# Kernel optimization log

Hardware: AMD Instinct MI355X
Metric: run time of the kernel (lower is better)

The kernel has to match this reference:

```python
import jax, jax.numpy as jnp
import numpy as np

B, C, HH, WW = 16, 512, 32, 32
NUM_HEADS = 8
NUM_GROUPS = 32
EPS = 1e-5


def setup_inputs() -> dict:
    key = jax.random.key(0)
    ks = jax.random.split(key, 4)
    x = jax.random.normal(ks[0], (B, C, HH, WW), dtype=jnp.float32)
    gn_scale = jnp.ones((C,), dtype=jnp.float32)
    gn_bias = jnp.zeros((C,), dtype=jnp.float32)
    qkv_w = jax.random.normal(ks[1], (3 * C, C), dtype=jnp.float32) * (1.0 / np.sqrt(C))
    qkv_b = jnp.zeros((3 * C,), dtype=jnp.float32)
    # NOTE: original zero-inits proj_out; we use random weights for a non-trivial baseline.
    proj_w = jax.random.normal(ks[2], (C, C), dtype=jnp.float32) * (1.0 / np.sqrt(C))
    proj_b = jnp.zeros((C,), dtype=jnp.float32)
    return {"x": x, "gn_scale": gn_scale, "gn_bias": gn_bias,
            "qkv_w": qkv_w, "qkv_b": qkv_b, "proj_w": proj_w, "proj_b": proj_b}


def reference(x, gn_scale, gn_bias, qkv_w, qkv_b, proj_w, proj_b):
    b, c, h, w = x.shape
    t = h * w
    nh = NUM_HEADS
    d = c // nh
    xf = x.reshape(b, c, t)                      # (B, C, T)

    # GroupNorm(32, C) over (channels-in-group, spatial)
    xg = xf.reshape(b, NUM_GROUPS, (c // NUM_GROUPS) * t)
    mu = jnp.mean(xg, axis=-1, keepdims=True)
    var = jnp.var(xg, axis=-1, keepdims=True)
    xn = ((xg - mu) * jax.lax.rsqrt(var + EPS)).reshape(b, c, t)
    xn = xn * gn_scale[:, None] + gn_bias[:, None]

    # 1x1 conv QKV: (3C, C) matmul over channel dim
    qkv = jnp.einsum('oc,bct->bot', qkv_w, xn) + qkv_b[:, None]
    # channel axis splits as (3, H, D) per rearrange 'B (three H C) T -> three B T H C'
    qkv = qkv.reshape(b, 3, nh, d, t)
    q, k, v = qkv[:, 0], qkv[:, 1], qkv[:, 2]    # each (B, H, D, T)

    scale = 1.0 / jnp.sqrt(jnp.asarray(d, x.dtype))
    logits = jnp.einsum('bhdt,bhds->bhts', q, k) * scale   # (B, H, T, S)
    probs = jax.nn.softmax(logits, axis=-1)
    attn = jnp.einsum('bhts,bhds->bhdt', probs, v)         # (B, H, D, T)

    hout = attn.reshape(b, c, t)                 # 'B T H C -> B (H C) T'
    hout = jnp.einsum('oc,bct->bot', proj_w, hout) + proj_b[:, None]
    return (hout + xf).reshape(b, c, h, w)
```

## Files before the change

### kernel.cpp

```cpp
#include <hip/hip_runtime.h>

typedef unsigned short ushort_t;
typedef unsigned int uint_t;
typedef __bf16 bf16x8 __attribute__((ext_vector_type(8)));
typedef float f32x4 __attribute__((ext_vector_type(4)));
typedef uint_t u32x4 __attribute__((ext_vector_type(4)));
typedef uint_t u32x2 __attribute__((ext_vector_type(2)));


static __device__ __forceinline__ ushort_t f2bf(float f) {
  union { float f; uint_t u; } v; v.f = f;
  uint_t r = v.u + 0x7FFFu + ((v.u >> 16) & 1u);
  return (ushort_t)(r >> 16);
}

static __device__ __forceinline__ uint_t cvt_pk_bf16(float lo, float hi) {
  uint_t r;
  asm("v_cvt_pk_bf16_f32 %0, %1, %2" : "=v"(r) : "v"(lo), "v"(hi));
  return r;
}

static __device__ __forceinline__ f32x4 mfma_bf16(bf16x8 a, bf16x8 b, f32x4 c) {
  return __builtin_amdgcn_mfma_f32_16x16x32_bf16(a, b, c, 0, 0, 0);
}

__global__ __launch_bounds__(256) void k_convert(const float* __restrict__ src,
                                                 ushort_t* __restrict__ dst, int n) {
  int i = (blockIdx.x * 256 + threadIdx.x) * 4;
  if (i >= n) return;
  f32x4 v = *(const f32x4*)(src + i);
  u32x2 o;
  o[0] = (uint_t)f2bf(v[0]) | ((uint_t)f2bf(v[1]) << 16);
  o[1] = (uint_t)f2bf(v[2]) | ((uint_t)f2bf(v[3]) << 16);
  *(u32x2*)(dst + i) = o;
}

__global__ __launch_bounds__(256) void k_gn(const float* __restrict__ x,
                                            const float* __restrict__ gsc,
                                            const float* __restrict__ gbi,
                                            ushort_t* __restrict__ xnT) {
  const int g = blockIdx.x, b = blockIdx.y;
  const int tid = threadIdx.x;
  const float* xp = x + ((size_t)b * 512 + g * 16) * 1024;

  float s = 0.f, q = 0.f;
#pragma unroll
  for (int i = 0; i < 16; ++i) {
    f32x4 v = *(const f32x4*)(xp + (tid + i * 256) * 4);
    s += v[0] + v[1] + v[2] + v[3];
    q += v[0]*v[0] + v[1]*v[1] + v[2]*v[2] + v[3]*v[3];
  }
#pragma unroll
  for (int off = 32; off > 0; off >>= 1) { s += __shfl_xor(s, off); q += __shfl_xor(q, off); }

  __shared__ float rs[4], rq[4], ssc[16], sbi[16], stats[2];
  if ((tid & 63) == 0) { rs[tid >> 6] = s; rq[tid >> 6] = q; }
  if (tid < 16) { ssc[tid] = gsc[g * 16 + tid]; sbi[tid] = gbi[g * 16 + tid]; }
  __syncthreads();
  if (tid == 0) {
    float S = rs[0] + rs[1] + rs[2] + rs[3];
    float Q = rq[0] + rq[1] + rq[2] + rq[3];
    float mean = S * (1.f / 16384.f);
    float var  = Q * (1.f / 16384.f) - mean * mean;
    stats[0] = mean; stats[1] = rsqrtf(var + 1e-5f);
  }
  __syncthreads();
  const float mean = stats[0], rstd = stats[1];

#pragma unroll
  for (int i = 0; i < 8; ++i) {
    int u = tid + i * 256;
    int t = u >> 1, half = u & 1;
    union { ushort_t us[8]; u32x4 v4; } o;
#pragma unroll
    for (int j = 0; j < 8; ++j) {
      int c = half * 8 + j;
      float v = (xp[(size_t)c * 1024 + t] - mean) * rstd * ssc[c] + sbi[c];
      o.us[j] = f2bf(v);
    }
    *(u32x4*)(xnT + ((size_t)b * 1024 + t) * 512 + g * 16 + half * 8) = o.v4;
  }
}

__global__ __launch_bounds__(256) void k_qkv(const ushort_t* __restrict__ xnT,
                                             const ushort_t* __restrict__ Wbf,
                                             const float* __restrict__ bias,
                                             ushort_t* __restrict__ qkT,
                                             ushort_t* __restrict__ vbuf) {
  const int mi = blockIdx.x, ni = blockIdx.y, b = blockIdx.z;
  const int tid = threadIdx.x, lane = tid & 63, w = tid >> 6;
  const int wm = w >> 1, wn = w & 1;
  const int lr = lane & 15, lg = lane >> 4;

  __shared__ __align__(16) ushort_t As[128 * 40];
  __shared__ __align__(16) ushort_t Bs[128 * 40];
  __shared__ __align__(16) float tbuf[32 * 132];

  const ushort_t* Ap = xnT + (size_t)b * 1024 * 512 + (size_t)mi * 128 * 512;
  const ushort_t* Bp = Wbf + (size_t)ni * 128 * 512;

  f32x4 acc[4][4] = {};

  for (int kt = 0; kt < 16; ++kt) {
    const int k0 = kt * 32;
#pragma unroll
    for (int uu = 0; uu < 2; ++uu) {
      const int u = tid + uu * 256;
      const int row = u >> 2, seg = u & 3;
      const u32x4 av = *(const u32x4*)(Ap + (size_t)row * 512 + k0 + seg * 8);
      const u32x4 bv = *(const u32x4*)(Bp + (size_t)row * 512 + k0 + seg * 8);
      *(u32x4*)(As + row * 40 + seg * 8) = av;
      *(u32x4*)(Bs + row * 40 + seg * 8) = bv;
    }
    __syncthreads();
    bf16x8 af[4], bfv[4];
#pragma unroll
    for (int i = 0; i < 4; ++i)
      af[i] = *(const bf16x8*)(As + (wm * 64 + i * 16 + lr) * 40 + lg * 8);
#pragma unroll
    for (int j = 0; j < 4; ++j)
      bfv[j] = *(const bf16x8*)(Bs + (wn * 64 + j * 16 + lr) * 40 + lg * 8);
    __builtin_amdgcn_s_setprio(1);
#pragma unroll
    for (int i = 0; i < 4; ++i)
#pragma unroll
      for (int j = 0; j < 4; ++j)
        acc[i][j] = mfma_bf16(af[i], bfv[j], acc[i][j]);
    __builtin_amdgcn_s_setprio(0);
    __syncthreads();
  }

  float biasv[4];
#pragma unroll
  for (int j = 0; j < 4; ++j) biasv[j] = bias[ni * 128 + wn * 64 + j * 16 + lr];

  if (ni < 8) {
    const float oscale = (ni >= 4) ? 0.1803368801f : 1.0f;
    ushort_t* outp = qkT + ((size_t)b * 1024 + mi * 128) * 1024 + ni * 128;
#pragma unroll
    for (int i = 0; i < 4; ++i)
#pragma unroll
      for (int j = 0; j < 4; ++j)
#pragma unroll
        for (int r = 0; r < 4; ++r) {
          const int m = wm * 64 + i * 16 + lg * 4 + r;
          const int n = wn * 64 + j * 16 + lr;
          outp[(size_t)m * 1024 + n] = f2bf((acc[i][j][r] + biasv[j]) * oscale);
        }
  } else {
    ushort_t* tb = (ushort_t*)tbuf;
#pragma unroll
    for (int c = 0; c < 4; ++c) {
      if (wn == (c >> 1)) {
#pragma unroll
        for (int jj = 0; jj < 2; ++jj) {
          const int j = (c & 1) * 2 + jj;
#pragma unroll
          for (int i = 0; i < 4; ++i)
#pragma unroll
            for (int r = 0; r < 4; ++r) {
              const int m = wm * 64 + i * 16 + lg * 4 + r;
              const int nl = jj * 16 + lr;
              tb[nl * 136 + m] = f2bf(acc[i][j][r] + biasv[j]);
            }
        }
      }
      __syncthreads();
      for (int u = tid; u < 512; u += 256) {
        const int nl = u >> 4, seg = u & 15;
        const int op = ni * 128 + c * 32 + nl - 1024;
        *(u32x4*)(vbuf + ((size_t)b * 512 + op) * 1024 + mi * 128 + seg * 8) =
            *(const u32x4*)(tb + nl * 136 + seg * 8);
      }
      __syncthreads();
    }
  }
}

#define PSTR 68
__global__ __launch_bounds__(256) void k_attn(const ushort_t* __restrict__ qkT,
                                              const ushort_t* __restrict__ vbuf,
                                              ushort_t* __restrict__ attnT) {
  const int qt = blockIdx.x, h = blockIdx.y, b = blockIdx.z;
  const int tid = threadIdx.x, lane = tid & 63, w = tid >> 6;
  const int lr = lane & 15, lg = lane >> 4;

  __shared__ __align__(16) ushort_t Ks[64 * PSTR];
  __shared__ __align__(16) ushort_t Vs[64 * PSTR];
  __shared__ __align__(16) ushort_t Ps[4 * 32 * PSTR];

  bf16x8 aq[2][2];
#pragma unroll
  for (int tI = 0; tI < 2; ++tI) {
    const int t = qt * 128 + w * 32 + tI * 16 + lr;
    const ushort_t* qp = qkT + ((size_t)b * 1024 + t) * 1024 + h * 64 + lg * 8;
    aq[tI][0] = *(const bf16x8*)(qp);
    aq[tI][1] = *(const bf16x8*)(qp + 32);
  }

  f32x4 oacc[2][4] = {};
  float lrun[2][4] = {};

  const size_t vbase = ((size_t)b * 512 + h * 64) * 1024;
  ushort_t* Pw = Ps + w * 32 * PSTR;

  for (int st = 0; st < 16; ++st) {
    const int s0 = st * 64;
    __syncthreads();
#pragma unroll
    for (int uu = 0; uu < 2; ++uu) {
      const int u = tid + uu * 256;
      const int row = u >> 3, seg = u & 7;
      const u32x4 kv = *(const u32x4*)(qkT + ((size_t)b * 1024 + s0 + row) * 1024 + 512 + h * 64 + seg * 8);
      const u32x4 vv = *(const u32x4*)(vbuf + vbase + (size_t)row * 1024 + s0 + seg * 8);
      *(u32x4*)(Ks + row * PSTR + seg * 8) = kv;
      *(u32x4*)(Vs + row * PSTR + seg * 8) = vv;
    }
    __syncthreads();

    f32x4 sacc[2][4] = {};
    __builtin_amdgcn_s_setprio(1);
#pragma unroll
    for (int sI = 0; sI < 4; ++sI) {
      const bf16x8 bk0 = *(const bf16x8*)(Ks + (sI * 16 + lr) * PSTR + lg * 8);
      const bf16x8 bk1 = *(const bf16x8*)(Ks + (sI * 16 + lr) * PSTR + 32 + lg * 8);
#pragma unroll
      for (int tI = 0; tI < 2; ++tI) {
        sacc[tI][sI] = mfma_bf16(aq[tI][0], bk0, sacc[tI][sI]);
        sacc[tI][sI] = mfma_bf16(aq[tI][1], bk1, sacc[tI][sI]);
      }
    }
    __builtin_amdgcn_s_setprio(0);

#pragma unroll
    for (int tI = 0; tI < 2; ++tI)
#pragma unroll
      for (int sI = 0; sI < 4; ++sI)
#pragma unroll
        for (int r = 0; r < 4; ++r)
          sacc[tI][sI][r] = __builtin_amdgcn_exp2f(sacc[tI][sI][r]);
#pragma unroll
    for (int tI = 0; tI < 2; ++tI)
#pragma unroll
      for (int r = 0; r < 4; ++r)
        lrun[tI][r] += (sacc[tI][0][r] + sacc[tI][1][r]) + (sacc[tI][2][r] + sacc[tI][3][r]);

#pragma unroll
    for (int tI = 0; tI < 2; ++tI)
#pragma unroll
      for (int r = 0; r < 4; ++r) {
        const int rb = (tI * 16 + lg * 4 + r) * PSTR;
        const uint_t u0 = cvt_pk_bf16(sacc[tI][0][r], sacc[tI][1][r]);
        const uint_t u1 = cvt_pk_bf16(sacc[tI][2][r], sacc[tI][3][r]);
        Pw[rb + lr]      = (ushort_t)u0;
        Pw[rb + lr + 16] = (ushort_t)(u0 >> 16);
        Pw[rb + lr + 32] = (ushort_t)u1;
        Pw[rb + lr + 48] = (ushort_t)(u1 >> 16);
      }

#pragma unroll
    for (int tI = 0; tI < 2; ++tI) {
      const bf16x8 ap0 = *(const bf16x8*)(Pw + (tI * 16 + lr) * PSTR + lg * 8);
      const bf16x8 ap1 = *(const bf16x8*)(Pw + (tI * 16 + lr) * PSTR + 32 + lg * 8);
      __builtin_amdgcn_s_setprio(1);
#pragma unroll
      for (int dI = 0; dI < 4; ++dI) {
        const bf16x8 bv0 = *(const bf16x8*)(Vs + (dI * 16 + lr) * PSTR + lg * 8);
        const bf16x8 bv1 = *(const bf16x8*)(Vs + (dI * 16 + lr) * PSTR + 32 + lg * 8);
        oacc[tI][dI] = mfma_bf16(ap0, bv0, oacc[tI][dI]);
        oacc[tI][dI] = mfma_bf16(ap1, bv1, oacc[tI][dI]);
      }
      __builtin_amdgcn_s_setprio(0);
    }
  }

  float inv[2][4];
#pragma unroll
  for (int tI = 0; tI < 2; ++tI)
#pragma unroll
    for (int r = 0; r < 4; ++r) {
      float sum = lrun[tI][r];
      sum += __shfl_xor(sum, 1);
      sum += __shfl_xor(sum, 2);
      sum += __shfl_xor(sum, 4);
      sum += __shfl_xor(sum, 8);
      inv[tI][r] = 1.f / sum;
    }
#pragma unroll
  for (int tI = 0; tI < 2; ++tI)
#pragma unroll
    for (int dI = 0; dI < 4; ++dI)
#pragma unroll
      for (int r = 0; r < 4; ++r) {
        const int t = qt * 128 + w * 32 + tI * 16 + lg * 4 + r;
        attnT[((size_t)b * 1024 + t) * 512 + h * 64 + dI * 16 + lr] =
            f2bf(oacc[tI][dI][r] * inv[tI][r]);
      }
}

__global__ __launch_bounds__(256) void k_proj(const ushort_t* __restrict__ attnT,
                                              const ushort_t* __restrict__ Wbf,
                                              const float* __restrict__ bias,
                                              const float* __restrict__ xres,
                                              float* __restrict__ outp) {
  const int mi = blockIdx.x, ni = blockIdx.y, b = blockIdx.z;
  const int tid = threadIdx.x, lane = tid & 63, w = tid >> 6;
  const int wm = w >> 1, wn = w & 1;
  const int lr = lane & 15, lg = lane >> 4;

  __shared__ __align__(16) ushort_t As[128 * 40];
  __shared__ __align__(16) ushort_t Bs[128 * 40];
  __shared__ __align__(16) float tbuf[32 * 132];

  const ushort_t* Ap = attnT + (size_t)b * 1024 * 512 + (size_t)mi * 128 * 512;
  const ushort_t* Bp = Wbf + (size_t)ni * 128 * 512;

  f32x4 acc[4][4] = {};

  for (int kt = 0; kt < 16; ++kt) {
    const int k0 = kt * 32;
#pragma unroll
    for (int uu = 0; uu < 2; ++uu) {
      const int u = tid + uu * 256;
      const int row = u >> 2, seg = u & 3;
      const u32x4 av = *(const u32x4*)(Ap + (size_t)row * 512 + k0 + seg * 8);
      const u32x4 bv = *(const u32x4*)(Bp + (size_t)row * 512 + k0 + seg * 8);
      *(u32x4*)(As + row * 40 + seg * 8) = av;
      *(u32x4*)(Bs + row * 40 + seg * 8) = bv;
    }
    __syncthreads();
    bf16x8 af[4], bfv[4];
#pragma unroll
    for (int i = 0; i < 4; ++i)
      af[i] = *(const bf16x8*)(As + (wm * 64 + i * 16 + lr) * 40 + lg * 8);
#pragma unroll
    for (int j = 0; j < 4; ++j)
      bfv[j] = *(const bf16x8*)(Bs + (wn * 64 + j * 16 + lr) * 40 + lg * 8);
    __builtin_amdgcn_s_setprio(1);
#pragma unroll
    for (int i = 0; i < 4; ++i)
#pragma unroll
      for (int j = 0; j < 4; ++j)
        acc[i][j] = mfma_bf16(af[i], bfv[j], acc[i][j]);
    __builtin_amdgcn_s_setprio(0);
    __syncthreads();
  }

  float biasv[4];
#pragma unroll
  for (int j = 0; j < 4; ++j) biasv[j] = bias[ni * 128 + wn * 64 + j * 16 + lr];

#pragma unroll
  for (int c = 0; c < 4; ++c) {
    if (wn == (c >> 1)) {
#pragma unroll
      for (int jj = 0; jj < 2; ++jj) {
        const int j = (c & 1) * 2 + jj;
#pragma unroll
        for (int i = 0; i < 4; ++i)
#pragma unroll
          for (int r = 0; r < 4; ++r) {
            const int m = wm * 64 + i * 16 + lg * 4 + r;
            const int nl = jj * 16 + lr;
            tbuf[nl * 132 + m] = acc[i][j][r] + biasv[j];
          }
      }
    }
    __syncthreads();
    for (int u = tid; u < 1024; u += 256) {
      const int nl = u >> 5, seg = u & 31;
      const int o = ni * 128 + c * 32 + nl;
      const size_t idx = ((size_t)b * 512 + o) * 1024 + mi * 128 + seg * 4;
      const f32x4 t = *(const f32x4*)(tbuf + nl * 132 + seg * 4);
      const f32x4 xr = *(const f32x4*)(xres + idx);
      f32x4 ov = t + xr;
      *(f32x4*)(outp + idx) = ov;
    }
    __syncthreads();
  }
}

extern "C" void kernel_launch(void* const* d_in, const int* in_sizes, int n_in,
                              void* d_out, int out_size, void* d_ws, size_t ws_size,
                              hipStream_t stream) {
  (void)in_sizes; (void)n_in; (void)out_size; (void)ws_size;
  const float* x      = (const float*)d_in[0];
  const float* gsc    = (const float*)d_in[1];
  const float* gbi    = (const float*)d_in[2];
  const float* qkv_w  = (const float*)d_in[3];
  const float* qkv_b  = (const float*)d_in[4];
  const float* proj_w = (const float*)d_in[5];
  const float* proj_b = (const float*)d_in[6];
  float* out = (float*)d_out;

  char* ws = (char*)d_ws;
  ushort_t* xnT   = (ushort_t*)(ws);
  ushort_t* qkT   = (ushort_t*)(ws + 16777216);
  ushort_t* vbuf  = (ushort_t*)(ws + 50331648);
  ushort_t* attnT = (ushort_t*)(ws + 67108864);
  ushort_t* qwbf  = (ushort_t*)(ws + 83886080);
  ushort_t* pwbf  = (ushort_t*)(ws + 85458944);

  k_convert<<<768, 256, 0, stream>>>(qkv_w, qwbf, 1536 * 512);
  k_convert<<<256, 256, 0, stream>>>(proj_w, pwbf, 512 * 512);
  k_gn<<<dim3(32, 16), 256, 0, stream>>>(x, gsc, gbi, xnT);
  k_qkv<<<dim3(8, 12, 16), 256, 0, stream>>>(xnT, qwbf, qkv_b, qkT, vbuf);
  k_attn<<<dim3(8, 8, 16), 256, 0, stream>>>(qkT, vbuf, attnT);
  k_proj<<<dim3(8, 4, 16), 256, 0, stream>>>(attnT, pwbf, proj_b, x, out);
}
```

Measured before the change: 256.7 us.

## Register-prefetch next K/V and GEMM tiles to overlap global loads with MFMA

In the QKV GEMM, attention and projection kernels, the next tile's global loads are issued into registers before the current tile's MFMA work and written to shared memory afterwards. This hides global memory latency behind compute using a single LDS buffer with two barriers per iteration. It costs extra vector registers per thread, which may reduce occupancy in the attention kernel.

```diff
diff --git a/kernel.cpp b/kernel.cpp
--- a/kernel.cpp
+++ b/kernel.cpp
@@ -99,20 +99,29 @@
   const ushort_t* Ap = xnT + (size_t)b * 1024 * 512 + (size_t)mi * 128 * 512;
   const ushort_t* Bp = Wbf + (size_t)ni * 128 * 512;
 
+  const int row0 = tid >> 2, seg = tid & 3;
+  u32x4 ra0, ra1, rb0, rb1;
+
+  ra0 = *(const u32x4*)(Ap + (size_t)row0 * 512 + seg * 8);
+  ra1 = *(const u32x4*)(Ap + (size_t)(row0 + 64) * 512 + seg * 8);
+  rb0 = *(const u32x4*)(Bp + (size_t)row0 * 512 + seg * 8);
+  rb1 = *(const u32x4*)(Bp + (size_t)(row0 + 64) * 512 + seg * 8);
+  *(u32x4*)(As + row0 * 40 + seg * 8) = ra0;
+  *(u32x4*)(As + (row0 + 64) * 40 + seg * 8) = ra1;
+  *(u32x4*)(Bs + row0 * 40 + seg * 8) = rb0;
+  *(u32x4*)(Bs + (row0 + 64) * 40 + seg * 8) = rb1;
+  __syncthreads();
+
   f32x4 acc[4][4] = {};
 
   for (int kt = 0; kt < 16; ++kt) {
-    const int k0 = kt * 32;
-#pragma unroll
-    for (int uu = 0; uu < 2; ++uu) {
-      const int u = tid + uu * 256;
-      const int row = u >> 2, seg = u & 3;
-      const u32x4 av = *(const u32x4*)(Ap + (size_t)row * 512 + k0 + seg * 8);
-      const u32x4 bv = *(const u32x4*)(Bp + (size_t)row * 512 + k0 + seg * 8);
-      *(u32x4*)(As + row * 40 + seg * 8) = av;
-      *(u32x4*)(Bs + row * 40 + seg * 8) = bv;
-    }
-    __syncthreads();
+    if (kt < 15) {
+      const int k0n = (kt + 1) * 32;
+      ra0 = *(const u32x4*)(Ap + (size_t)row0 * 512 + k0n + seg * 8);
+      ra1 = *(const u32x4*)(Ap + (size_t)(row0 + 64) * 512 + k0n + seg * 8);
+      rb0 = *(const u32x4*)(Bp + (size_t)row0 * 512 + k0n + seg * 8);
+      rb1 = *(const u32x4*)(Bp + (size_t)(row0 + 64) * 512 + k0n + seg * 8);
+    }
     bf16x8 af[4], bfv[4];
 #pragma unroll
     for (int i = 0; i < 4; ++i)
@@ -127,7 +136,14 @@
       for (int j = 0; j < 4; ++j)
         acc[i][j] = mfma_bf16(af[i], bfv[j], acc[i][j]);
     __builtin_amdgcn_s_setprio(0);
-    __syncthreads();
+    if (kt < 15) {
+      __syncthreads();
+      *(u32x4*)(As + row0 * 40 + seg * 8) = ra0;
+      *(u32x4*)(As + (row0 + 64) * 40 + seg * 8) = ra1;
+      *(u32x4*)(Bs + row0 * 40 + seg * 8) = rb0;
+      *(u32x4*)(Bs + (row0 + 64) * 40 + seg * 8) = rb1;
+      __syncthreads();
+    }
   }
 
   float biasv[4];
@@ -167,10 +183,10 @@
       }
       __syncthreads();
       for (int u = tid; u < 512; u += 256) {
-        const int nl = u >> 4, seg = u & 15;
+        const int nl = u >> 4, sg = u & 15;
         const int op = ni * 128 + c * 32 + nl - 1024;
-        *(u32x4*)(vbuf + ((size_t)b * 512 + op) * 1024 + mi * 128 + seg * 8) =
-            *(const u32x4*)(tb + nl * 136 + seg * 8);
+        *(u32x4*)(vbuf + ((size_t)b * 512 + op) * 1024 + mi * 128 + sg * 8) =
+            *(const u32x4*)(tb + nl * 136 + sg * 8);
       }
       __syncthreads();
     }
@@ -202,21 +218,30 @@
   float lrun[2][4] = {};
 
   const size_t vbase = ((size_t)b * 512 + h * 64) * 1024;
+  const size_t kbase = (size_t)b * 1024 * 1024 + 512 + h * 64;
   ushort_t* Pw = Ps + w * 32 * PSTR;
 
+  const int srow = tid >> 3, sseg = tid & 7;
+  u32x4 kr0, kr1, vr0, vr1;
+
+  kr0 = *(const u32x4*)(qkT + kbase + (size_t)srow * 1024 + sseg * 8);
+  kr1 = *(const u32x4*)(qkT + kbase + (size_t)(srow + 32) * 1024 + sseg * 8);
+  vr0 = *(const u32x4*)(vbuf + vbase + (size_t)srow * 1024 + sseg * 8);
+  vr1 = *(const u32x4*)(vbuf + vbase + (size_t)(srow + 32) * 1024 + sseg * 8);
+  *(u32x4*)(Ks + srow * PSTR + sseg * 8) = kr0;
+  *(u32x4*)(Ks + (srow + 32) * PSTR + sseg * 8) = kr1;
+  *(u32x4*)(Vs + srow * PSTR + sseg * 8) = vr0;
+  *(u32x4*)(Vs + (srow + 32) * PSTR + sseg * 8) = vr1;
+  __syncthreads();
+
   for (int st = 0; st < 16; ++st) {
-    const int s0 = st * 64;
-    __syncthreads();
-#pragma unroll
-    for (int uu = 0; uu < 2; ++uu) {
-      const int u = tid + uu * 256;
-      const int row = u >> 3, seg = u & 7;
-      const u32x4 kv = *(const u32x4*)(qkT + ((size_t)b * 1024 + s0 + row) * 1024 + 512 + h * 64 + seg * 8);
-      const u32x4 vv = *(const u32x4*)(vbuf + vbase + (size_t)row * 1024 + s0 + seg * 8);
-      *(u32x4*)(Ks + row * PSTR + seg * 8) = kv;
-      *(u32x4*)(Vs + row * PSTR + seg * 8) = vv;
-    }
-    __syncthreads();
+    if (st < 15) {
+      const int s0n = (st + 1) * 64;
+      kr0 = *(const u32x4*)(qkT + kbase + (size_t)(s0n + srow) * 1024 + sseg * 8);
+      kr1 = *(const u32x4*)(qkT + kbase + (size_t)(s0n + srow + 32) * 1024 + sseg * 8);
+      vr0 = *(const u32x4*)(vbuf + vbase + (size_t)srow * 1024 + s0n + sseg * 8);
+      vr1 = *(const u32x4*)(vbuf + vbase + (size_t)(srow + 32) * 1024 + s0n + sseg * 8);
+    }
 
     f32x4 sacc[2][4] = {};
     __builtin_amdgcn_s_setprio(1);
@@ -271,6 +296,15 @@
         oacc[tI][dI] = mfma_bf16(ap1, bv1, oacc[tI][dI]);
       }
       __builtin_amdgcn_s_setprio(0);
+    }
+
+    if (st < 15) {
+      __syncthreads();
+      *(u32x4*)(Ks + srow * PSTR + sseg * 8) = kr0;
+      *(u32x4*)(Ks + (srow + 32) * PSTR + sseg * 8) = kr1;
+      *(u32x4*)(Vs + srow * PSTR + sseg * 8) = vr0;
+      *(u32x4*)(Vs + (srow + 32) * PSTR + sseg * 8) = vr1;
+      __syncthreads();
     }
   }
 
@@ -315,20 +349,29 @@
   const ushort_t* Ap = attnT + (size_t)b * 1024 * 512 + (size_t)mi * 128 * 512;
   const ushort_t* Bp = Wbf + (size_t)ni * 128 * 512;
 
+  const int row0 = tid >> 2, seg = tid & 3;
+  u32x4 ra0, ra1, rb0, rb1;
+
+  ra0 = *(const u32x4*)(Ap + (size_t)row0 * 512 + seg * 8);
+  ra1 = *(const u32x4*)(Ap + (size_t)(row0 + 64) * 512 + seg * 8);
+  rb0 = *(const u32x4*)(Bp + (size_t)row0 * 512 + seg * 8);
+  rb1 = *(const u32x4*)(Bp + (size_t)(row0 + 64) * 512 + seg * 8);
+  *(u32x4*)(As + row0 * 40 + seg * 8) = ra0;
+  *(u32x4*)(As + (row0 + 64) * 40 + seg * 8) = ra1;
+  *(u32x4*)(Bs + row0 * 40 + seg * 8) = rb0;
+  *(u32x4*)(Bs + (row0 + 64) * 40 + seg * 8) = rb1;
+  __syncthreads();
+
   f32x4 acc[4][4] = {};
 
   for (int kt = 0; kt < 16; ++kt) {
-    const int k0 = kt * 32;
-#pragma unroll
-    for (int uu = 0; uu < 2; ++uu) {
-      const int u = tid + uu * 256;
-      const int row = u >> 2, seg = u & 3;
-      const u32x4 av = *(const u32x4*)(Ap + (size_t)row * 512 + k0 + seg * 8);
-      const u32x4 bv = *(const u32x4*)(Bp + (size_t)row * 512 + k0 + seg * 8);
-      *(u32x4*)(As + row * 40 + seg * 8) = av;
-      *(u32x4*)(Bs + row * 40 + seg * 8) = bv;
-    }
-    __syncthreads();
+    if (kt < 15) {
+      const int k0n = (kt + 1) * 32;
+      ra0 = *(const u32x4*)(Ap + (size_t)row0 * 512 + k0n + seg * 8);
+      ra1 = *(const u32x4*)(Ap + (size_t)(row0 + 64) * 512 + k0n + seg * 8);
+      rb0 = *(const u32x4*)(Bp + (size_t)row0 * 512 + k0n + seg * 8);
+      rb1 = *(const u32x4*)(Bp + (size_t)(row0 + 64) * 512 + k0n + seg * 8);
+    }
     bf16x8 af[4], bfv[4];
 #pragma unroll
     for (int i = 0; i < 4; ++i)
@@ -343,7 +386,14 @@
       for (int j = 0; j < 4; ++j)
         acc[i][j] = mfma_bf16(af[i], bfv[j], acc[i][j]);
     __builtin_amdgcn_s_setprio(0);
-    __syncthreads();
+    if (kt < 15) {
+      __syncthreads();
+      *(u32x4*)(As + row0 * 40 + seg * 8) = ra0;
+      *(u32x4*)(As + (row0 + 64) * 40 + seg * 8) = ra1;
+      *(u32x4*)(Bs + row0 * 40 + seg * 8) = rb0;
+      *(u32x4*)(Bs + (row0 + 64) * 40 + seg * 8) = rb1;
+      __syncthreads();
+    }
   }
 
   float biasv[4];
@@ -368,10 +418,10 @@
     }
     __syncthreads();
     for (int u = tid; u < 1024; u += 256) {
-      const int nl = u >> 5, seg = u & 31;
+      const int nl = u >> 5, sg = u & 31;
       const int o = ni * 128 + c * 32 + nl;
-      const size_t idx = ((size_t)b * 512 + o) * 1024 + mi * 128 + seg * 4;
-      const f32x4 t = *(const f32x4*)(tbuf + nl * 132 + seg * 4);
+      const size_t idx = ((size_t)b * 512 + o) * 1024 + mi * 128 + sg * 4;
+      const f32x4 t = *(const f32x4*)(tbuf + nl * 132 + sg * 4);
       const f32x4 xr = *(const f32x4*)(xres + idx);
       f32x4 ov = t + xr;
       *(f32x4*)(outp + idx) = ov;
```

Result: faster. 247.5 us (-3.6%).
